# Performance work log

Measured on AMD Instinct MI355X. Metric: run time of the kernel, lower is better.

Reference implementation:

```python
import jax, jax.numpy as jnp
import numpy as np

DECAY = 0.99
EPS = 1e-5
COMMITMENT_COST = 0.25


def setup_inputs() -> dict:
    key = jax.random.key(0)
    k1, k2, k3, k4 = jax.random.split(key, 4)
    N, D, K = 262144, 128, 512
    return {
        "z": jax.random.normal(k1, (N, D), dtype=jnp.float32),
        "embedding": jax.random.normal(k2, (K, D), dtype=jnp.float32),
        "ema_cluster_size": jax.random.uniform(k3, (K,), dtype=jnp.float32),
        "ema_w": jax.random.normal(k4, (K, D), dtype=jnp.float32),
    }


def reference(z, embedding, ema_cluster_size, ema_w):
    # EMA-based VectorQuantizer forward (training mode), matching torch source.
    D = z.shape[-1]
    K = embedding.shape[0]
    flat_z = z.reshape(-1, D)  # [N, D]

    # ||z||^2 + ||e||^2 - 2 z.e  -> [N, K]
    distances = (
        jnp.sum(flat_z * flat_z, axis=1, keepdims=True)
        + jnp.sum(embedding * embedding, axis=1)
        - 2.0 * flat_z @ embedding.T
    )
    indices = jnp.argmin(distances, axis=1)  # [N]

    # one_hot @ embedding == gather (same math, no dense [N,K] one-hot)
    z_q = embedding[indices]  # [N, D]

    # EMA buffer updates (torch does these on buffers / .data, no grads)
    counts = jax.ops.segment_sum(jnp.ones_like(indices, dtype=flat_z.dtype), indices, num_segments=K)
    new_ema_cluster_size = ema_cluster_size * DECAY + (1.0 - DECAY) * counts
    dw = jax.ops.segment_sum(flat_z, indices, num_segments=K)  # encodings.T @ flat_z
    new_ema_w = ema_w * DECAY + (1.0 - DECAY) * dw
    n = jnp.sum(new_ema_cluster_size)
    cluster_size = (new_ema_cluster_size + EPS) / (n + K * EPS) * n
    new_embedding = new_ema_w / cluster_size[:, None]

    loss = COMMITMENT_COST * jnp.mean((jax.lax.stop_gradient(z_q) - flat_z) ** 2)
    # straight-through estimator
    z_q_st = flat_z + jax.lax.stop_gradient(z_q - flat_z)
    z_q_st = z_q_st.reshape(z.shape)
    return (z_q_st, loss, indices, new_ema_cluster_size, new_ema_w, new_embedding)
```

## Files before the change

### kernel.cpp

```cpp
#include <hip/hip_runtime.h>

#define NPTS 262144
#define DIM 128
#define KCL 512

constexpr float DECAY = 0.99f;
constexpr float EPSV = 1e-5f;
constexpr float CCOST = 0.25f;

#define O_ZQ 0
#define O_LOSS (NPTS * DIM)
#define O_IDX (O_LOSS + 1)
#define O_NECS (O_IDX + NPTS)
#define O_NEMAW (O_NECS + KCL)
#define O_NEMB (O_NEMAW + KCL * DIM)

#define W_ENORM 0
#define W_COUNTS 512
#define W_LOSS 1024
#define W_NFLAG 1025
#define W_NFLAG2 1026
#define W_DW 1088
#define W_CS 66624
#define W_OFF 67136
#define W_CUR 67712
#define W_EHI 68224
#define W_FLAG2 100992
#define FLAG2CAP 4096
#define W_FLAG 109184
#define FLAGCAP 45056
#define W_IDX 199296
#define W_SORTED (W_IDX + NPTS)

#define MARGIN 0.25f
#define MARGIN2 0.005f
#define SEG 64
#define RB 16

using v8h = __attribute__((ext_vector_type(8))) _Float16;
using v4f = __attribute__((ext_vector_type(4))) float;

__global__ void k_prep(const float* __restrict__ emb,
                       unsigned short* __restrict__ ehi,
                       float* __restrict__ wsf) {
    __shared__ float part[4][16];
    const int t = threadIdx.x;
    const int g = blockIdx.x;
    const int lane = t & 63, ks = t >> 6;
    const int col = lane & 15, quad = lane >> 4;
    const float* src = emb + (size_t)(g * 16 + col) * DIM + ks * 32 + quad * 8;
    float4 a = *(const float4*)src;
    float4 b = *(const float4*)(src + 4);
    float f[8] = {a.x, a.y, a.z, a.w, b.x, b.y, b.z, b.w};
    union { unsigned short s[8]; int4 v; } uh;
    float s2 = 0.0f;
#pragma unroll
    for (int j = 0; j < 8; j++) {
        _Float16 h = (_Float16)f[j];
        uh.s[j] = __builtin_bit_cast(unsigned short, h);
        s2 += f[j] * f[j];
    }
    *(int4*)&ehi[((size_t)g * 256 + t) * 8] = uh.v;
    s2 += __shfl_xor(s2, 16);
    s2 += __shfl_xor(s2, 32);
    if (quad == 0) part[ks][col] = s2;
    __syncthreads();
    if (t < 16)
        wsf[W_ENORM + g * 16 + t] = part[0][t] + part[1][t] + part[2][t] + part[3][t];
}

__global__ __launch_bounds__(512, 2) void k_main(
    const float* __restrict__ z, const float* __restrict__ emb,
    const unsigned short* __restrict__ ehi,
    float* __restrict__ out, float* __restrict__ wsf,
    unsigned* __restrict__ wsu, int* __restrict__ wsi) {
    __shared__ short seh[KCL * DIM];
    __shared__ float sen[KCL];
    __shared__ int   ishs[256];

    const int t = threadIdx.x;
    const int blk = blockIdx.x;
    const int w = t >> 6;
    const int lane = t & 63;
    const int col = lane & 15;
    const int quad = lane >> 4;

    int4 stg[16];
    {
        const int4* src = (const int4*)ehi;
#pragma unroll
        for (int i = 0; i < 16; i++) stg[i] = src[t + 512 * i];
    }
    sen[t] = wsf[W_ENORM + t];

    v8h ah[2][4], al[2][4];
    float zn[2];
#pragma unroll
    for (int mt = 0; mt < 2; mt++) {
        zn[mt] = 0.0f;
        const float* zr = z + (size_t)(blk * 256 + w * 32 + mt * 16 + col) * DIM;
#pragma unroll
        for (int ks = 0; ks < 4; ks++) {
            const float* p = zr + ks * 32 + quad * 8;
            float4 a = *(const float4*)p;
            float4 b = *(const float4*)(p + 4);
            float f[8] = {a.x, a.y, a.z, a.w, b.x, b.y, b.z, b.w};
#pragma unroll
            for (int j = 0; j < 8; j++) {
                _Float16 h = (_Float16)f[j];
                float r = f[j] - (float)h;
                ah[mt][ks][j] = h;
                al[mt][ks][j] = (_Float16)r;
                zn[mt] += f[j] * f[j];
            }
        }
        zn[mt] += __shfl_xor(zn[mt], 16);
        zn[mt] += __shfl_xor(zn[mt], 32);
    }

#pragma unroll
    for (int i = 0; i < 16; i++) ((int4*)seh)[t + 512 * i] = stg[i];
    __syncthreads();

    float rv1[8], rv2[8];
    int ri1[8];
#pragma unroll
    for (int s = 0; s < 8; s++) { rv1[s] = 3.4e38f; rv2[s] = 3.4e38f; ri1[s] = 0; }

#pragma unroll 2
    for (int g = 0; g < 32; g++) {
        v8h bh[4];
#pragma unroll
        for (int ks = 0; ks < 4; ks++)
            bh[ks] = *(const v8h*)&seh[((g * 4 + ks) * 64 + lane) * 8];
        v4f acc0 = {0.f, 0.f, 0.f, 0.f}, acc1 = {0.f, 0.f, 0.f, 0.f};
#pragma unroll
        for (int ks = 0; ks < 4; ks++) {
            acc0 = __builtin_amdgcn_mfma_f32_16x16x32_f16(ah[0][ks], bh[ks], acc0, 0, 0, 0);
            acc1 = __builtin_amdgcn_mfma_f32_16x16x32_f16(ah[1][ks], bh[ks], acc1, 0, 0, 0);
        }
#pragma unroll
        for (int ks = 0; ks < 4; ks++) {
            acc0 = __builtin_amdgcn_mfma_f32_16x16x32_f16(al[0][ks], bh[ks], acc0, 0, 0, 0);
            acc1 = __builtin_amdgcn_mfma_f32_16x16x32_f16(al[1][ks], bh[ks], acc1, 0, 0, 0);
        }
        const int kbase = g * 16 + col;
        const float en = sen[kbase];
#pragma unroll
        for (int mt = 0; mt < 2; mt++)
#pragma unroll
            for (int r = 0; r < 4; r++) {
                int s = mt * 4 + r;
                float dist = fmaf(-2.0f, (mt ? acc1[r] : acc0[r]), en);
                bool better = dist < rv1[s];
                rv2[s] = fminf(fmaxf(dist, rv1[s]), rv2[s]);
                rv1[s] = better ? dist : rv1[s];
                ri1[s] = better ? kbase : ri1[s];
            }
    }

#pragma unroll
    for (int m = 1; m < 16; m <<= 1) {
#pragma unroll
        for (int s = 0; s < 8; s++) {
            float c1 = __shfl_xor(rv1[s], m);
            int ci1 = __shfl_xor(ri1[s], m);
            float c2 = __shfl_xor(rv2[s], m);
            if (c1 < rv1[s] || (c1 == rv1[s] && ci1 < ri1[s])) {
                rv2[s] = fminf(rv1[s], c2);
                rv1[s] = c1; ri1[s] = ci1;
            } else {
                rv2[s] = fminf(rv2[s], c1);
            }
        }
    }

    float znp[8];
#pragma unroll
    for (int s = 0; s < 8; s++) znp[s] = __shfl(zn[s >> 2], quad * 4 + (s & 3));

    float lossacc = 0.0f;
    if (col == 0) {
#pragma unroll
        for (int s = 0; s < 8; s++) {
            int p = w * 32 + (s >> 2) * 16 + quad * 4 + (s & 3);
            int gp = blk * 256 + p;
            float v1 = rv1[s]; int i1 = ri1[s];
            float fd = v1 + znp[s];
            out[O_IDX + gp] = (float)i1;
            wsi[W_IDX + gp] = i1;
            ishs[p] = i1;
            atomicAdd(&wsu[W_COUNTS + i1], 1u);
            lossacc += fd;
            if (rv2[s] - v1 < MARGIN) {
                unsigned pos = atomicAdd(&wsu[W_NFLAG], 1u);
                if (pos < FLAGCAP) {
                    wsu[W_FLAG + 2 * pos] = (unsigned)gp;
                    wsu[W_FLAG + 2 * pos + 1] = __float_as_uint(fd);
                }
            }
        }
    }
    for (int o = 32; o > 0; o >>= 1) lossacc += __shfl_down(lossacc, o);
    if (lane == 0) atomicAdd(&wsf[W_LOSS], lossacc);

    __syncthreads();
    float* outz = out + (size_t)blk * 256 * DIM;
#pragma unroll
    for (int i = 0; i < 16; i++) {
        int f4 = t + 512 * i;
        int p = f4 >> 5, dq = f4 & 31;
        int ci = ishs[p];
        float4 v = *(const float4*)(emb + (size_t)ci * DIM + 4 * dq);
        ((float4*)outz)[f4] = v;
    }
}

__global__ __launch_bounds__(256) void k_recheck1(
    const float* __restrict__ z, const float* __restrict__ emb,
    float* __restrict__ out, float* __restrict__ wsf,
    unsigned* __restrict__ wsu, int* __restrict__ wsi) {
    __shared__ float zs[RB][DIM];
    __shared__ float zns[RB];
    __shared__ unsigned sgp[RB];
    __shared__ float sfd[RB];
    __shared__ float r1[RB][257];
    __shared__ float r2[RB][257];
    __shared__ int   rix[RB][257];
    const int t = threadIdx.x;
    unsigned nf = wsu[W_NFLAG];
    if (nf > FLAGCAP) nf = FLAGCAP;
    unsigned nb = (nf + RB - 1) / RB;
    for (unsigned b = blockIdx.x; b < nb; b += gridDim.x) {
        __syncthreads();
        if (t < RB) {
            unsigned fi = b * RB + t;
            if (fi < nf) {
                sgp[t] = wsu[W_FLAG + 2 * fi];
                sfd[t] = __uint_as_float(wsu[W_FLAG + 2 * fi + 1]);
            } else { sgp[t] = 0u; sfd[t] = 0.0f; }
        }
        __syncthreads();
        {
            int p = t >> 4, j = t & 15;
            const float4* src = (const float4*)(z + (size_t)sgp[p] * DIM);
            *(float4*)&zs[p][j * 8] = src[j * 2];
            *(float4*)&zs[p][j * 8 + 4] = src[j * 2 + 1];
        }
        __syncthreads();
        if (t < RB) {
            float s = 0.0f;
            for (int d = 0; d < DIM; d += 4) {
                float4 v = *(const float4*)&zs[t][d];
                s += v.x * v.x + v.y * v.y + v.z * v.z + v.w * v.w;
            }
            zns[t] = s;
        }
        float acc0[RB], acc1[RB];
#pragma unroll
        for (int p = 0; p < RB; p++) { acc0[p] = 0.0f; acc1[p] = 0.0f; }
        const float4* e0 = (const float4*)(emb + (size_t)(2 * t) * DIM);
        const float4* e1 = (const float4*)(emb + (size_t)(2 * t + 1) * DIM);
#pragma unroll 2
        for (int ch = 0; ch < 32; ch++) {
            float4 ea = e0[ch], eb = e1[ch];
#pragma unroll
            for (int p = 0; p < RB; p++) {
                float4 zv = *(const float4*)&zs[p][ch * 4];
                acc0[p] = fmaf(zv.x, ea.x, fmaf(zv.y, ea.y, fmaf(zv.z, ea.z, fmaf(zv.w, ea.w, acc0[p]))));
                acc1[p] = fmaf(zv.x, eb.x, fmaf(zv.y, eb.y, fmaf(zv.z, eb.z, fmaf(zv.w, eb.w, acc1[p]))));
            }
        }
        float en0 = wsf[W_ENORM + 2 * t];
        float en1 = wsf[W_ENORM + 2 * t + 1];
#pragma unroll
        for (int p = 0; p < RB; p++) {
            float d0 = fmaf(-2.0f, acc0[p], en0);
            float d1 = fmaf(-2.0f, acc1[p], en1);
            float v1 = d0, v2 = d1; int i1 = 2 * t;
            if (d1 < d0) { v1 = d1; i1 = 2 * t + 1; v2 = d0; }
            r1[p][t] = v1; rix[p][t] = i1; r2[p][t] = v2;
        }
        __syncthreads();
        {
            int p = t >> 4, j = t & 15;
            float v1 = 3.4e38f, v2 = 3.4e38f; int i1 = 0x7fffffff;
#pragma unroll
            for (int k = 0; k < 16; k++) {
                int idx = j + 16 * k;
                float c1 = r1[p][idx]; int ci = rix[p][idx]; float c2 = r2[p][idx];
                if (c1 < v1 || (c1 == v1 && ci < i1)) { v2 = fminf(v1, c2); v1 = c1; i1 = ci; }
                else v2 = fminf(v2, c1);
            }
#pragma unroll
            for (int m = 1; m < 16; m <<= 1) {
                float c1 = __shfl_xor(v1, m);
                int ci = __shfl_xor(i1, m);
                float c2 = __shfl_xor(v2, m);
                if (c1 < v1 || (c1 == v1 && ci < i1)) { v2 = fminf(v1, c2); v1 = c1; i1 = ci; }
                else v2 = fminf(v2, c1);
            }
            bool valid = (b * RB + (unsigned)p < nf);
            unsigned gp = sgp[p];
            int chg = 0;
            if (j == 0 && valid) {
                if (v2 - v1 < MARGIN2) {
                    unsigned pos = atomicAdd(&wsu[W_NFLAG2], 1u);
                    if (pos < FLAG2CAP) {
                        wsu[W_FLAG2 + 2 * pos] = gp;
                        wsu[W_FLAG2 + 2 * pos + 1] = __float_as_uint(sfd[p]);
                    }
                } else {
                    float d = v1 + zns[p];
                    atomicAdd(&wsf[W_LOSS], d - sfd[p]);
                    int iold = wsi[W_IDX + gp];
                    if (i1 != iold) {
                        chg = 1;
                        wsi[W_IDX + gp] = i1;
                        out[O_IDX + gp] = (float)i1;
                        atomicAdd(&wsu[W_COUNTS + iold], (unsigned)-1);
                        atomicAdd(&wsu[W_COUNTS + i1], 1u);
                    }
                }
            }
            chg = __shfl(chg, (t & 63) & ~15);
            if (chg) {
                int dd = j * 8;
                *(float4*)&out[(size_t)gp * DIM + dd] =
                    *(const float4*)&emb[(size_t)i1 * DIM + dd];
                *(float4*)&out[(size_t)gp * DIM + dd + 4] =
                    *(const float4*)&emb[(size_t)i1 * DIM + dd + 4];
            }
        }
    }
}

__global__ __launch_bounds__(256) void k_recheck2(
    const float* __restrict__ z, const float* __restrict__ emb,
    float* __restrict__ out, float* __restrict__ wsf,
    unsigned* __restrict__ wsu, int* __restrict__ wsi) {
    __shared__ float zrow[DIM];
    __shared__ double sd[256];
    __shared__ int si[256];
    __shared__ int schg, snew;
    const int t = threadIdx.x;
    unsigned nf = wsu[W_NFLAG2];
    if (nf > FLAG2CAP) nf = FLAG2CAP;
    for (unsigned fi = blockIdx.x; fi < nf; fi += gridDim.x) {
        unsigned gp = wsu[W_FLAG2 + 2 * fi];
        float fd_prov = __uint_as_float(wsu[W_FLAG2 + 2 * fi + 1]);
        __syncthreads();
        if (t < DIM) zrow[t] = z[(size_t)gp * DIM + t];
        __syncthreads();
        double best = 1e300; int bi = 0;
        for (int c = t; c < KCL; c += 256) {
            const float* er = emb + (size_t)c * DIM;
            double d = 0.0;
            for (int dd = 0; dd < DIM; dd++) {
                double df = (double)zrow[dd] - (double)er[dd];
                d += df * df;
            }
            if (d < best) { best = d; bi = c; }
        }
        sd[t] = best; si[t] = bi;
        __syncthreads();
        for (int o = 128; o > 0; o >>= 1) {
            if (t < o) {
                if (sd[t + o] < sd[t] || (sd[t + o] == sd[t] && si[t + o] < si[t])) {
                    sd[t] = sd[t + o]; si[t] = si[t + o];
                }
            }
            __syncthreads();
        }
        if (t == 0) {
            int inew = si[0];
            int iold = wsi[W_IDX + gp];
            snew = inew;
            schg = (inew != iold);
            atomicAdd(&wsf[W_LOSS], (float)sd[0] - fd_prov);
            if (inew != iold) {
                wsi[W_IDX + gp] = inew;
                out[O_IDX + gp] = (float)inew;
                atomicAdd(&wsu[W_COUNTS + iold], (unsigned)-1);
                atomicAdd(&wsu[W_COUNTS + inew], 1u);
            }
        }
        __syncthreads();
        if (schg && t < DIM) out[(size_t)gp * DIM + t] = emb[(size_t)snew * DIM + t];
        __syncthreads();
    }
}

__global__ void k_finalize(const float* __restrict__ ema_cs, float* __restrict__ out,
                           float* __restrict__ wsf, unsigned* __restrict__ wsu) {
    __shared__ float s[KCL];
    __shared__ unsigned sc[KCL];
    int t = threadIdx.x;
    unsigned c = wsu[W_COUNTS + t];
    float necs = ema_cs[t] * DECAY + (1.0f - DECAY) * (float)c;
    out[O_NECS + t] = necs;
    s[t] = necs;
    __syncthreads();
    for (int o = 256; o > 0; o >>= 1) {
        if (t < o) s[t] += s[t + o];
        __syncthreads();
    }
    float n = s[0];
    float cs = (necs + EPSV) / (n + (float)KCL * EPSV) * n;
    wsf[W_CS + t] = cs;
    sc[t] = c;
    __syncthreads();
    for (int o = 1; o < KCL; o <<= 1) {
        unsigned v = (t >= o) ? sc[t - o] : 0u;
        __syncthreads();
        sc[t] += v;
        __syncthreads();
    }
    unsigned excl = sc[t] - c;
    wsu[W_OFF + t] = excl;
    wsu[W_CUR + t] = excl;
    if (t == 0) {
        out[O_LOSS] = CCOST * wsf[W_LOSS] / (float)((size_t)NPTS * DIM);
        wsu[W_OFF + KCL] = NPTS;
    }
}

__global__ void k_scatter(unsigned* __restrict__ wsu, const int* __restrict__ wsi) {
    int p = blockIdx.x * blockDim.x + threadIdx.x;
    int k = wsi[W_IDX + p];
    unsigned pos = atomicAdd(&wsu[W_CUR + k], 1u);
    wsu[W_SORTED + pos] = (unsigned)p;
}

__global__ __launch_bounds__(256) void k_dwseg(
    const float* __restrict__ z, float* __restrict__ wsf,
    const unsigned* __restrict__ wsu) {
    __shared__ unsigned soff[KCL + 1];
    __shared__ unsigned sidx[SEG];
    const int t = threadIdx.x;
    for (int i = t; i < KCL + 1; i += 256) soff[i] = wsu[W_OFF + i];
    const int base = blockIdx.x * SEG;
    if (t < SEG) sidx[t] = wsu[W_SORTED + base + t];
    __syncthreads();

    const int r = t >> 7;
    const int d = t & 127;
    const int pos0 = base + r;
    int lo = 0, hi = KCL;
    while (lo < hi) {
        int mid = (lo + hi + 1) >> 1;
        if (soff[mid] <= (unsigned)pos0) lo = mid; else hi = mid - 1;
    }
    int curk = lo;
    float acc = 0.0f;
#pragma unroll 4
    for (int j = 0; j < SEG / 2; j++) {
        int pos = pos0 + 2 * j;
        unsigned p = sidx[pos - base];
        while ((unsigned)pos >= soff[curk + 1]) {
            if (acc != 0.0f) atomicAdd(&wsf[W_DW + curk * DIM + d], acc);
            acc = 0.0f;
            curk++;
        }
        acc += z[(size_t)p * DIM + d];
    }
    atomicAdd(&wsf[W_DW + curk * DIM + d], acc);
}

__global__ void k_emb(const float* __restrict__ ema_w, float* __restrict__ out,
                      const float* __restrict__ wsf) {
    int i = blockIdx.x * 256 + threadIdx.x;
    int k = i >> 7;
    float dw = wsf[W_DW + i];
    float nw = ema_w[i] * DECAY + (1.0f - DECAY) * dw;
    out[O_NEMAW + i] = nw;
    out[O_NEMB + i] = nw / wsf[W_CS + k];
}

extern "C" void kernel_launch(void* const* d_in, const int* in_sizes, int n_in,
                              void* d_out, int out_size, void* d_ws, size_t ws_size,
                              hipStream_t stream) {
    const float* z = (const float*)d_in[0];
    const float* emb = (const float*)d_in[1];
    const float* ema_cs = (const float*)d_in[2];
    const float* ema_w = (const float*)d_in[3];
    float* out = (float*)d_out;
    float* wsf = (float*)d_ws;
    unsigned* wsu = (unsigned*)d_ws;
    int* wsi = (int*)d_ws;
    unsigned short* ehi = (unsigned short*)(wsu + W_EHI);

    hipMemsetAsync((char*)d_ws + (size_t)W_COUNTS * 4, 0,
                   (size_t)(W_DW + KCL * DIM - W_COUNTS) * 4, stream);

    k_prep<<<32, 256, 0, stream>>>(emb, ehi, wsf);
    k_main<<<NPTS / 256, 512, 0, stream>>>(z, emb, ehi, out, wsf, wsu, wsi);
    k_recheck1<<<512, 256, 0, stream>>>(z, emb, out, wsf, wsu, wsi);
    k_recheck2<<<256, 256, 0, stream>>>(z, emb, out, wsf, wsu, wsi);
    k_finalize<<<1, KCL, 0, stream>>>(ema_cs, out, wsf, wsu);
    k_scatter<<<NPTS / 256, 256, 0, stream>>>(wsu, wsi);
    k_dwseg<<<NPTS / SEG, 256, 0, stream>>>(z, wsf, wsu);
    k_emb<<<KCL * DIM / 256, 256, 0, stream>>>(ema_w, out, wsf);
}
```

Before: 843.9 us.

## Stream codebook through double-buffered LDS tiles and drop fp16 residual MFMAs

The main kernel moves to 128-point blocks of 256 threads. Instead of holding the whole fp16 codebook in 128 KB of shared memory, it streams 64-code tiles through two 16 KB buffers, loading the next tile into registers while computing the current one. This lowers shared memory per block so more blocks fit per CU and global loads overlap with MFMA work. It also removes the low-part fp16 residual of z, which halves the MFMA count but makes the distances less accurate. That risks more near-tie points, or wrong argmins if the fixed recheck margin no longer covers the larger error.

```diff
diff --git a/kernel.cpp b/kernel.cpp
--- a/kernel.cpp
+++ b/kernel.cpp
@@ -69,14 +69,14 @@
         wsf[W_ENORM + g * 16 + t] = part[0][t] + part[1][t] + part[2][t] + part[3][t];
 }
 
-__global__ __launch_bounds__(512, 2) void k_main(
+__global__ __launch_bounds__(256, 4) void k_main(
     const float* __restrict__ z, const float* __restrict__ emb,
     const unsigned short* __restrict__ ehi,
     float* __restrict__ out, float* __restrict__ wsf,
     unsigned* __restrict__ wsu, int* __restrict__ wsi) {
-    __shared__ short seh[KCL * DIM];
+    __shared__ short sbuf[2][8192];
     __shared__ float sen[KCL];
-    __shared__ int   ishs[256];
+    __shared__ int   ishs[128];
 
     const int t = threadIdx.x;
     const int blk = blockIdx.x;
@@ -85,20 +85,22 @@
     const int col = lane & 15;
     const int quad = lane >> 4;
 
-    int4 stg[16];
+    sen[t] = wsf[W_ENORM + t];
+    sen[t + 256] = wsf[W_ENORM + t + 256];
+
+    int4 stg[4];
     {
         const int4* src = (const int4*)ehi;
 #pragma unroll
-        for (int i = 0; i < 16; i++) stg[i] = src[t + 512 * i];
-    }
-    sen[t] = wsf[W_ENORM + t];
-
-    v8h ah[2][4], al[2][4];
+        for (int i = 0; i < 4; i++) stg[i] = src[t + 256 * i];
+    }
+
+    v8h ah[2][4];
     float zn[2];
 #pragma unroll
     for (int mt = 0; mt < 2; mt++) {
         zn[mt] = 0.0f;
-        const float* zr = z + (size_t)(blk * 256 + w * 32 + mt * 16 + col) * DIM;
+        const float* zr = z + (size_t)(blk * 128 + w * 32 + mt * 16 + col) * DIM;
 #pragma unroll
         for (int ks = 0; ks < 4; ks++) {
             const float* p = zr + ks * 32 + quad * 8;
@@ -107,10 +109,7 @@
             float f[8] = {a.x, a.y, a.z, a.w, b.x, b.y, b.z, b.w};
 #pragma unroll
             for (int j = 0; j < 8; j++) {
-                _Float16 h = (_Float16)f[j];
-                float r = f[j] - (float)h;
-                ah[mt][ks][j] = h;
-                al[mt][ks][j] = (_Float16)r;
+                ah[mt][ks][j] = (_Float16)f[j];
                 zn[mt] += f[j] * f[j];
             }
         }
@@ -119,7 +118,7 @@
     }
 
 #pragma unroll
-    for (int i = 0; i < 16; i++) ((int4*)seh)[t + 512 * i] = stg[i];
+    for (int i = 0; i < 4; i++) ((int4*)sbuf[0])[t + 256 * i] = stg[i];
     __syncthreads();
 
     float rv1[8], rv2[8];
@@ -127,36 +126,45 @@
 #pragma unroll
     for (int s = 0; s < 8; s++) { rv1[s] = 3.4e38f; rv2[s] = 3.4e38f; ri1[s] = 0; }
 
-#pragma unroll 2
-    for (int g = 0; g < 32; g++) {
-        v8h bh[4];
-#pragma unroll
-        for (int ks = 0; ks < 4; ks++)
-            bh[ks] = *(const v8h*)&seh[((g * 4 + ks) * 64 + lane) * 8];
-        v4f acc0 = {0.f, 0.f, 0.f, 0.f}, acc1 = {0.f, 0.f, 0.f, 0.f};
-#pragma unroll
-        for (int ks = 0; ks < 4; ks++) {
-            acc0 = __builtin_amdgcn_mfma_f32_16x16x32_f16(ah[0][ks], bh[ks], acc0, 0, 0, 0);
-            acc1 = __builtin_amdgcn_mfma_f32_16x16x32_f16(ah[1][ks], bh[ks], acc1, 0, 0, 0);
-        }
-#pragma unroll
-        for (int ks = 0; ks < 4; ks++) {
-            acc0 = __builtin_amdgcn_mfma_f32_16x16x32_f16(al[0][ks], bh[ks], acc0, 0, 0, 0);
-            acc1 = __builtin_amdgcn_mfma_f32_16x16x32_f16(al[1][ks], bh[ks], acc1, 0, 0, 0);
-        }
-        const int kbase = g * 16 + col;
-        const float en = sen[kbase];
-#pragma unroll
-        for (int mt = 0; mt < 2; mt++)
-#pragma unroll
-            for (int r = 0; r < 4; r++) {
-                int s = mt * 4 + r;
-                float dist = fmaf(-2.0f, (mt ? acc1[r] : acc0[r]), en);
-                bool better = dist < rv1[s];
-                rv2[s] = fminf(fmaxf(dist, rv1[s]), rv2[s]);
-                rv1[s] = better ? dist : rv1[s];
-                ri1[s] = better ? kbase : ri1[s];
-            }
+    for (int kt = 0; kt < 8; kt++) {
+        const short* bcur = sbuf[kt & 1];
+        if (kt < 7) {
+            const int4* src = (const int4*)ehi + (kt + 1) * 1024;
+#pragma unroll
+            for (int i = 0; i < 4; i++) stg[i] = src[t + 256 * i];
+        }
+#pragma unroll
+        for (int g = 0; g < 4; g++) {
+            v8h bh[4];
+#pragma unroll
+            for (int ks = 0; ks < 4; ks++)
+                bh[ks] = *(const v8h*)&bcur[((g * 4 + ks) * 64 + lane) * 8];
+            v4f acc0 = {0.f, 0.f, 0.f, 0.f}, acc1 = {0.f, 0.f, 0.f, 0.f};
+#pragma unroll
+            for (int ks = 0; ks < 4; ks++) {
+                acc0 = __builtin_amdgcn_mfma_f32_16x16x32_f16(ah[0][ks], bh[ks], acc0, 0, 0, 0);
+                acc1 = __builtin_amdgcn_mfma_f32_16x16x32_f16(ah[1][ks], bh[ks], acc1, 0, 0, 0);
+            }
+            const int kbase = (kt * 4 + g) * 16 + col;
+            const float en = sen[kbase];
+#pragma unroll
+            for (int mt = 0; mt < 2; mt++)
+#pragma unroll
+                for (int r = 0; r < 4; r++) {
+                    int s = mt * 4 + r;
+                    float dist = fmaf(-2.0f, (mt ? acc1[r] : acc0[r]), en);
+                    bool better = dist < rv1[s];
+                    rv2[s] = fminf(fmaxf(dist, rv1[s]), rv2[s]);
+                    rv1[s] = better ? dist : rv1[s];
+                    ri1[s] = better ? kbase : ri1[s];
+                }
+        }
+        if (kt < 7) {
+            short* bnxt = sbuf[(kt & 1) ^ 1];
+#pragma unroll
+            for (int i = 0; i < 4; i++) ((int4*)bnxt)[t + 256 * i] = stg[i];
+        }
+        __syncthreads();
     }
 
 #pragma unroll
@@ -184,7 +192,7 @@
 #pragma unroll
         for (int s = 0; s < 8; s++) {
             int p = w * 32 + (s >> 2) * 16 + quad * 4 + (s & 3);
-            int gp = blk * 256 + p;
+            int gp = blk * 128 + p;
             float v1 = rv1[s]; int i1 = ri1[s];
             float fd = v1 + znp[s];
             out[O_IDX + gp] = (float)i1;
@@ -205,10 +213,10 @@
     if (lane == 0) atomicAdd(&wsf[W_LOSS], lossacc);
 
     __syncthreads();
-    float* outz = out + (size_t)blk * 256 * DIM;
+    float* outz = out + (size_t)blk * 128 * DIM;
 #pragma unroll
     for (int i = 0; i < 16; i++) {
-        int f4 = t + 512 * i;
+        int f4 = t + 256 * i;
         int p = f4 >> 5, dq = f4 & 31;
         int ci = ishs[p];
         float4 v = *(const float4*)(emb + (size_t)ci * DIM + 4 * dq);
@@ -494,7 +502,7 @@
                    (size_t)(W_DW + KCL * DIM - W_COUNTS) * 4, stream);
 
     k_prep<<<32, 256, 0, stream>>>(emb, ehi, wsf);
-    k_main<<<NPTS / 256, 512, 0, stream>>>(z, emb, ehi, out, wsf, wsu, wsi);
+    k_main<<<NPTS / 128, 256, 0, stream>>>(z, emb, ehi, out, wsf, wsu, wsi);
     k_recheck1<<<512, 256, 0, stream>>>(z, emb, out, wsf, wsu, wsi);
     k_recheck2<<<256, 256, 0, stream>>>(z, emb, out, wsf, wsu, wsi);
     k_finalize<<<1, KCL, 0, stream>>>(ema_cs, out, wsf, wsu);
```

New measurement: 858.3 us. No clear change (+1.7%).
